# Optimization experiments

Hardware: AMD Instinct MI355X
Metric: run time of the kernel (lower is better)

Reference implementation:

```python
import jax, jax.numpy as jnp
import numpy as np
import math

D_MODEL = 1024
N_HEADS = 16
HEAD_DIM = D_MODEL // N_HEADS
WINDOW = 256
LN_EPS = 1e-5


def _layernorm(x, g, b):
    mu = jnp.mean(x, axis=-1, keepdims=True)
    var = jnp.var(x, axis=-1, keepdims=True)
    return (x - mu) * jax.lax.rsqrt(var + LN_EPS) * g + b


def _window_mask(L):
    # row i attends to columns [i - W//2, i + W//2] inclusive; -inf elsewhere
    i = jnp.arange(L)[:, None]
    j = jnp.arange(L)[None, :]
    inside = (j >= i - WINDOW // 2) & (j <= i + WINDOW // 2)
    return jnp.where(inside, 0.0, -jnp.inf)  # [L, L]


def setup_inputs() -> dict:
    key = jax.random.key(0)
    ks = jax.random.split(key, 6)
    B, L, D = 2, 2048, D_MODEL
    s = 0.02
    return {
        "x": jax.random.normal(ks[0], (B, L, D), jnp.float32),
        "qkv_w": jax.random.normal(ks[1], (D, 3 * D), jnp.float32) * s,
        "qkv_b": jnp.zeros((3 * D,), jnp.float32),
        "out_w": jax.random.normal(ks[2], (D, D), jnp.float32) * s,
        "out_b": jnp.zeros((D,), jnp.float32),
        "ln1_g": jnp.ones((D,), jnp.float32),
        "ln1_b": jnp.zeros((D,), jnp.float32),
        "ln2_g": jnp.ones((D,), jnp.float32),
        "ln2_b": jnp.zeros((D,), jnp.float32),
        "ffn_w1": jax.random.normal(ks[3], (D, 2 * D), jnp.float32) * s,
        "ffn_b1": jnp.zeros((2 * D,), jnp.float32),
        "ffn_w2": jax.random.normal(ks[4], (2 * D, D), jnp.float32) * s,
        "ffn_b2": jnp.zeros((D,), jnp.float32),
    }


def reference(x, qkv_w, qkv_b, out_w, out_b, ln1_g, ln1_b, ln2_g, ln2_b,
              ffn_w1, ffn_b1, ffn_w2, ffn_b2):
    B, L, D = x.shape
    # --- sparse (windowed) attention on LN1(x) ---
    h = _layernorm(x, ln1_g, ln1_b)
    qkv = h @ qkv_w + qkv_b                       # [B, L, 3D]
    qkv = qkv.reshape(B, L, 3, N_HEADS, HEAD_DIM)
    q = qkv[:, :, 0].transpose(0, 2, 1, 3)        # [B, H, L, hd]
    k = qkv[:, :, 1].transpose(0, 2, 1, 3)
    v = qkv[:, :, 2].transpose(0, 2, 1, 3)
    scores = jnp.einsum('bhqd,bhkd->bhqk', q, k) / math.sqrt(HEAD_DIM)
    scores = scores + _window_mask(L)             # broadcast [L,L] over [B,H]
    attn = jax.nn.softmax(scores, axis=-1)
    out = jnp.einsum('bhqk,bhkd->bhqd', attn, v)  # [B, H, L, hd]
    out = out.transpose(0, 2, 1, 3).reshape(B, L, D)
    attn_out = out @ out_w + out_b
    x = x + attn_out
    # --- FFN on LN2(x) ---
    h2 = _layernorm(x, ln2_g, ln2_b)
    ffn = jax.nn.gelu(h2 @ ffn_w1 + ffn_b1, approximate=False) @ ffn_w2 + ffn_b2
    return x + ffn
```

## Files before the change

### kernel.cpp

```cpp
#include <hip/hip_runtime.h>
#include <hip/hip_bf16.h>

#define D_MODEL 1024
#define L_SEQ   2048
#define BATCH   2
#define NROWS   (BATCH*L_SEQ)
#define N_HEADS 16
#define HD      64
#define WIN     128

typedef __attribute__((ext_vector_type(8))) short short8;
typedef __attribute__((ext_vector_type(4))) float f32x4;
typedef __attribute__((ext_vector_type(4))) int   i32x4;
typedef __attribute__((ext_vector_type(4))) unsigned short u16x4;

__device__ __forceinline__ float bf2f(unsigned short u) {
  union { unsigned int i; float f; } c;
  c.i = ((unsigned int)u) << 16;
  return c.f;
}
__device__ __forceinline__ unsigned short f2bf(float f) {
  __hip_bfloat16 h = __float2bfloat16(f);
  return *reinterpret_cast<unsigned short*>(&h);
}

__global__ __launch_bounds__(256) void wtrans_kernel(const float* __restrict__ W,
                                                     __hip_bfloat16* __restrict__ Wt,
                                                     int K, int N) {
  __shared__ float tile[32][33];
  int tx = threadIdx.x & 31, ty = threadIdx.x >> 5;
  int n0 = blockIdx.x * 32, k0 = blockIdx.y * 32;
#pragma unroll
  for (int i = 0; i < 4; ++i) {
    int k = k0 + ty + i * 8;
    tile[ty + i * 8][tx] = W[(size_t)k * N + n0 + tx];
  }
  __syncthreads();
#pragma unroll
  for (int i = 0; i < 4; ++i) {
    int n = n0 + ty + i * 8;
    Wt[(size_t)n * K + k0 + tx] = __float2bfloat16(tile[tx][ty + i * 8]);
  }
}

__global__ __launch_bounds__(256) void vtrans_kernel(const __hip_bfloat16* __restrict__ qkv,
                                                     __hip_bfloat16* __restrict__ vT) {
  __shared__ unsigned short tile[64][72];
  int bh = blockIdx.y, b = bh >> 4, h = bh & 15;
  int j0 = blockIdx.x * 64;
  int t = threadIdx.x;
#pragma unroll
  for (int i = 0; i < 2; ++i) {
    int c = t + i * 256;
    int row = c >> 3, off = c & 7;
    *(i32x4*)&tile[row][off * 8] =
        *(const i32x4*)&qkv[(size_t)(b * L_SEQ + j0 + row) * 3072 + 2 * D_MODEL + h * 64 + off * 8];
  }
  __syncthreads();
#pragma unroll
  for (int i = 0; i < 2; ++i) {
    int c = t + i * 256;
    int d = c >> 3, off = c & 7;
    short8 o;
#pragma unroll
    for (int e = 0; e < 8; ++e) o[e] = (short)tile[off * 8 + e][d];
    *(short8*)&vT[((size_t)bh * 64 + d) * 2048 + j0 + off * 8] = o;
  }
}

__global__ __launch_bounds__(256) void ln_kernel(const float* __restrict__ x,
                                                 const float* __restrict__ g,
                                                 const float* __restrict__ beta,
                                                 __hip_bfloat16* __restrict__ out) {
  int row = blockIdx.x;
  int t = threadIdx.x;
  const float4* xr = (const float4*)(x + (size_t)row * D_MODEL);
  float4 v = xr[t];
  float s  = v.x + v.y + v.z + v.w;
  float sq = v.x * v.x + v.y * v.y + v.z * v.z + v.w * v.w;
#pragma unroll
  for (int off = 32; off; off >>= 1) {
    s  += __shfl_xor(s, off);
    sq += __shfl_xor(sq, off);
  }
  __shared__ float red[8];
  int w = t >> 6;
  if ((t & 63) == 0) { red[w] = s; red[4 + w] = sq; }
  __syncthreads();
  s  = red[0] + red[1] + red[2] + red[3];
  sq = red[4] + red[5] + red[6] + red[7];
  float mean = s * (1.0f / 1024.0f);
  float var  = sq * (1.0f / 1024.0f) - mean * mean;
  float rs   = rsqrtf(var + 1e-5f);
  float4 gv = ((const float4*)g)[t];
  float4 bv = ((const float4*)beta)[t];
  u16x4 o;
  o.x = f2bf((v.x - mean) * rs * gv.x + bv.x);
  o.y = f2bf((v.y - mean) * rs * gv.y + bv.y);
  o.z = f2bf((v.z - mean) * rs * gv.z + bv.z);
  o.w = f2bf((v.w - mean) * rs * gv.w + bv.w);
  ((u16x4*)(out + (size_t)row * D_MODEL))[t] = o;
}

template <int MODE>
__global__ __launch_bounds__(256) void gemm_kernel(const __hip_bfloat16* __restrict__ A,
                                                   const __hip_bfloat16* __restrict__ Bt,
                                                   const float* __restrict__ bias,
                                                   const float* __restrict__ resid,
                                                   void* __restrict__ outp,
                                                   int M, int N, int K) {
  (void)M;
  __shared__ char lsA[128 * 128];
  __shared__ char lsB[128 * 128];

  int tid  = threadIdx.x;
  int lane = tid & 63;
  int wave = tid >> 6;
  int wr = wave >> 1, wc = wave & 1;

  int m0 = blockIdx.y * 128;
  int n0 = blockIdx.x * 128;

  const char* Abase = (const char*)A;
  const char* Bbase = (const char*)Bt;
  size_t strideK = (size_t)K * 2;
  int KT = K >> 6;

  int srow = tid >> 3;
  int skb  = (tid & 7) * 16;

  f32x4 zero = {0.f, 0.f, 0.f, 0.f};
  f32x4 acc[4][4];
#pragma unroll
  for (int i = 0; i < 4; ++i)
#pragma unroll
    for (int j = 0; j < 4; ++j) acc[i][j] = zero;

  i32x4 ra[4], rb[4];
#pragma unroll
  for (int c = 0; c < 4; ++c) {
    int row = srow + c * 32;
    ra[c] = *(const i32x4*)(Abase + (size_t)(m0 + row) * strideK + skb);
    rb[c] = *(const i32x4*)(Bbase + (size_t)(n0 + row) * strideK + skb);
  }
#pragma unroll
  for (int c = 0; c < 4; ++c) {
    int row = srow + c * 32;
    int kb  = skb ^ ((row & 7) << 4);
    *(i32x4*)(lsA + row * 128 + kb) = ra[c];
    *(i32x4*)(lsB + row * 128 + kb) = rb[c];
  }
  __syncthreads();

  for (int kt = 0; kt < KT; ++kt) {
    if (kt + 1 < KT) {
#pragma unroll
      for (int c = 0; c < 4; ++c) {
        int row = srow + c * 32;
        ra[c] = *(const i32x4*)(Abase + (size_t)(m0 + row) * strideK + (size_t)(kt + 1) * 128 + skb);
        rb[c] = *(const i32x4*)(Bbase + (size_t)(n0 + row) * strideK + (size_t)(kt + 1) * 128 + skb);
      }
    }
#pragma unroll
    for (int ks = 0; ks < 2; ++ks) {
      short8 af[4], bfr[4];
#pragma unroll
      for (int mi = 0; mi < 4; ++mi) {
        int row = wr * 64 + mi * 16 + (lane & 15);
        int kb  = (ks * 64 + ((lane >> 4) << 4)) ^ ((row & 7) << 4);
        af[mi] = *(const short8*)(lsA + row * 128 + kb);
      }
#pragma unroll
      for (int ni = 0; ni < 4; ++ni) {
        int row = wc * 64 + ni * 16 + (lane & 15);
        int kb  = (ks * 64 + ((lane >> 4) << 4)) ^ ((row & 7) << 4);
        bfr[ni] = *(const short8*)(lsB + row * 128 + kb);
      }
#pragma unroll
      for (int mi = 0; mi < 4; ++mi)
#pragma unroll
        for (int ni = 0; ni < 4; ++ni)
          acc[mi][ni] = __builtin_amdgcn_mfma_f32_16x16x32_bf16(af[mi], bfr[ni], acc[mi][ni], 0, 0, 0);
    }
    __syncthreads();
    if (kt + 1 < KT) {
#pragma unroll
      for (int c = 0; c < 4; ++c) {
        int row = srow + c * 32;
        int kb  = skb ^ ((row & 7) << 4);
        *(i32x4*)(lsA + row * 128 + kb) = ra[c];
        *(i32x4*)(lsB + row * 128 + kb) = rb[c];
      }
    }
    __syncthreads();
  }

  int colg = n0 + wc * 64;
  int rowg = m0 + wr * 64;
#pragma unroll
  for (int mi = 0; mi < 4; ++mi) {
#pragma unroll
    for (int ni = 0; ni < 4; ++ni) {
      int col = colg + ni * 16 + (lane & 15);
      float bs = bias[col];
#pragma unroll
      for (int r = 0; r < 4; ++r) {
        int row = rowg + mi * 16 + ((lane >> 4) << 2) + r;
        float v = acc[mi][ni][r] + bs;
        if (MODE == 1) v = 0.5f * v * (1.0f + erff(v * 0.70710678118654752f));
        if (MODE == 2) {
          ((float*)outp)[(size_t)row * N + col] = v + resid[(size_t)row * N + col];
        } else {
          ((__hip_bfloat16*)outp)[(size_t)row * N + col] = __float2bfloat16(v);
        }
      }
    }
  }
}

__global__ __launch_bounds__(256) void attn_mfma_kernel(const __hip_bfloat16* __restrict__ qkv,
                                                        const __hip_bfloat16* __restrict__ vT,
                                                        __hip_bfloat16* __restrict__ out) {
  __shared__ char Ks[2][8192];
  __shared__ char Vs[2][8192];
  __shared__ char Ps[4][2304];

  const int t = threadIdx.x;
  const int lane = t & 63;
  const int wave = t >> 6;
  const int l15 = lane & 15;
  const int lg  = lane >> 4;
  const int bh = blockIdx.y, b = bh >> 4, h = bh & 15;
  const int q0 = blockIdx.x * 64;
  const int jlo = q0 - 128;

  short8 qf0, qf1;
  {
    int qrow = q0 + wave * 16 + l15;
    const char* qp = (const char*)qkv + 2 * ((size_t)(b * L_SEQ + qrow) * 3072 + h * 64 + 8 * lg);
    qf0 = *(const short8*)qp;
    qf1 = *(const short8*)(qp + 64);
  }

  const int srow = t >> 3;
  const int soff = (t & 7) * 16;
  const int jel  = (t & 7) * 8;

  const char* kgbase = (const char*)qkv + 2 * ((size_t)b * L_SEQ * 3072 + D_MODEL + h * 64);
  const char* vgbase = (const char*)vT + 2 * ((size_t)bh * 64 * 2048);

  f32x4 sc[5][4];
#pragma unroll
  for (int c = 0; c < 5; ++c)
#pragma unroll
    for (int tt = 0; tt < 4; ++tt) sc[c][tt] = (f32x4){0.f, 0.f, 0.f, 0.f};

  {
    i32x4 kr[2];
#pragma unroll
    for (int i = 0; i < 2; ++i) {
      int rr = srow + i * 32;
      int tok = jlo + rr; tok = tok < 0 ? 0 : (tok > 2047 ? 2047 : tok);
      kr[i] = *(const i32x4*)(kgbase + (size_t)tok * 6144 + soff);
    }
#pragma unroll
    for (int i = 0; i < 2; ++i) {
      int rr = srow + i * 32;
      *(i32x4*)(Ks[0] + rr * 128 + (soff ^ ((rr & 7) << 4))) = kr[i];
    }
  }
  __syncthreads();

#pragma unroll
  for (int c = 0; c < 5; ++c) {
    int cur = c & 1;
    i32x4 nk[2];
    if (c < 4) {
#pragma unroll
      for (int i = 0; i < 2; ++i) {
        int rr = srow + i * 32;
        int tok = jlo + (c + 1) * 64 + rr; tok = tok < 0 ? 0 : (tok > 2047 ? 2047 : tok);
        nk[i] = *(const i32x4*)(kgbase + (size_t)tok * 6144 + soff);
      }
    }
#pragma unroll
    for (int tt = 0; tt < 4; ++tt) {
      int row = tt * 16 + l15;
      short8 k0 = *(const short8*)(Ks[cur] + row * 128 + ((lg * 16) ^ ((row & 7) << 4)));
      short8 k1 = *(const short8*)(Ks[cur] + row * 128 + ((64 + lg * 16) ^ ((row & 7) << 4)));
      sc[c][tt] = __builtin_amdgcn_mfma_f32_16x16x32_bf16(qf0, k0, sc[c][tt], 0, 0, 0);
      sc[c][tt] = __builtin_amdgcn_mfma_f32_16x16x32_bf16(qf1, k1, sc[c][tt], 0, 0, 0);
    }
    if (c < 4) {
      __syncthreads();
#pragma unroll
      for (int i = 0; i < 2; ++i) {
        int rr = srow + i * 32;
        *(i32x4*)(Ks[cur ^ 1] + rr * 128 + (soff ^ ((rr & 7) << 4))) = nk[i];
      }
      __syncthreads();
    }
  }

  const int iqb = q0 + wave * 16 + 4 * lg;
  const int kgb = jlo + l15;
#pragma unroll
  for (int c = 0; c < 5; ++c)
#pragma unroll
    for (int tt = 0; tt < 4; ++tt) {
      int kg = kgb + c * 64 + tt * 16;
#pragma unroll
      for (int r = 0; r < 4; ++r) {
        int iq = iqb + r;
        bool ok = (kg >= 0) && (kg < L_SEQ) && (kg >= iq - WIN) && (kg <= iq + WIN);
        sc[c][tt][r] = ok ? sc[c][tt][r] * 0.125f : -1e30f;
      }
    }
  float mx[4] = {-1e30f, -1e30f, -1e30f, -1e30f};
#pragma unroll
  for (int c = 0; c < 5; ++c)
#pragma unroll
    for (int tt = 0; tt < 4; ++tt)
#pragma unroll
      for (int r = 0; r < 4; ++r) mx[r] = fmaxf(mx[r], sc[c][tt][r]);
#pragma unroll
  for (int r = 0; r < 4; ++r)
#pragma unroll
    for (int off = 8; off; off >>= 1) mx[r] = fmaxf(mx[r], __shfl_xor(mx[r], off, 16));
  float sm[4] = {0.f, 0.f, 0.f, 0.f};
#pragma unroll
  for (int c = 0; c < 5; ++c)
#pragma unroll
    for (int tt = 0; tt < 4; ++tt)
#pragma unroll
      for (int r = 0; r < 4; ++r) {
        float p = __expf(sc[c][tt][r] - mx[r]);
        sc[c][tt][r] = p;
        sm[r] += p;
      }
#pragma unroll
  for (int r = 0; r < 4; ++r)
#pragma unroll
    for (int off = 8; off; off >>= 1) sm[r] += __shfl_xor(sm[r], off, 16);
  float inv[4];
#pragma unroll
  for (int r = 0; r < 4; ++r) inv[r] = 1.f / sm[r];
#pragma unroll
  for (int c = 0; c < 5; ++c)
#pragma unroll
    for (int tt = 0; tt < 4; ++tt)
#pragma unroll
      for (int r = 0; r < 4; ++r) sc[c][tt][r] *= inv[r];

  f32x4 o[4];
#pragma unroll
  for (int dt = 0; dt < 4; ++dt) o[dt] = (f32x4){0.f, 0.f, 0.f, 0.f};

  {
    i32x4 vr[2];
#pragma unroll
    for (int i = 0; i < 2; ++i) {
      int rr = srow + i * 32;
      int js = jlo + jel; js = js < 0 ? 0 : (js > 2040 ? 2040 : js);
      vr[i] = *(const i32x4*)(vgbase + 2 * ((size_t)rr * 2048 + js));
    }
    __syncthreads();
#pragma unroll
    for (int i = 0; i < 2; ++i) {
      int rr = srow + i * 32;
      *(i32x4*)(Vs[0] + rr * 128 + (soff ^ ((rr & 7) << 4))) = vr[i];
    }
  }
  __syncthreads();

  char* pw = Ps[wave];
#pragma unroll
  for (int c = 0; c < 5; ++c) {
    int cur = c & 1;
    i32x4 nv[2];
    if (c < 4) {
#pragma unroll
      for (int i = 0; i < 2; ++i) {
        int rr = srow + i * 32;
        int js = jlo + (c + 1) * 64 + jel; js = js < 0 ? 0 : (js > 2040 ? 2040 : js);
        nv[i] = *(const i32x4*)(vgbase + 2 * ((size_t)rr * 2048 + js));
      }
    }
#pragma unroll
    for (int tt = 0; tt < 4; ++tt)
#pragma unroll
      for (int r = 0; r < 4; ++r)
        *(unsigned short*)(pw + (4 * lg + r) * 144 + (tt * 16 + l15) * 2) = f2bf(sc[c][tt][r]);
    short8 pa0 = *(const short8*)(pw + l15 * 144 + lg * 16);
    short8 pa1 = *(const short8*)(pw + l15 * 144 + 64 + lg * 16);
#pragma unroll
    for (int dt = 0; dt < 4; ++dt) {
      int row = dt * 16 + l15;
      short8 v0 = *(const short8*)(Vs[cur] + row * 128 + ((lg * 16) ^ ((row & 7) << 4)));
      short8 v1 = *(const short8*)(Vs[cur] + row * 128 + ((64 + lg * 16) ^ ((row & 7) << 4)));
      o[dt] = __builtin_amdgcn_mfma_f32_16x16x32_bf16(pa0, v0, o[dt], 0, 0, 0);
      o[dt] = __builtin_amdgcn_mfma_f32_16x16x32_bf16(pa1, v1, o[dt], 0, 0, 0);
    }
    if (c < 4) {
      __syncthreads();
#pragma unroll
      for (int i = 0; i < 2; ++i) {
        int rr = srow + i * 32;
        *(i32x4*)(Vs[cur ^ 1] + rr * 128 + (soff ^ ((rr & 7) << 4))) = nv[i];
      }
      __syncthreads();
    }
  }

  char* ob = (char*)out + 2 * ((size_t)(b * L_SEQ + q0 + wave * 16) * D_MODEL + h * 64);
#pragma unroll
  for (int dt = 0; dt < 4; ++dt)
#pragma unroll
    for (int r = 0; r < 4; ++r)
      *(unsigned short*)(ob + 2 * ((size_t)(4 * lg + r) * D_MODEL + dt * 16 + l15)) = f2bf(o[dt][r]);
}

extern "C" void kernel_launch(void* const* d_in, const int* in_sizes, int n_in,
                              void* d_out, int out_size, void* d_ws, size_t ws_size,
                              hipStream_t stream) {
  const float* x      = (const float*)d_in[0];
  const float* qkv_w  = (const float*)d_in[1];
  const float* qkv_b  = (const float*)d_in[2];
  const float* out_w  = (const float*)d_in[3];
  const float* out_b  = (const float*)d_in[4];
  const float* ln1_g  = (const float*)d_in[5];
  const float* ln1_b  = (const float*)d_in[6];
  const float* ln2_g  = (const float*)d_in[7];
  const float* ln2_b  = (const float*)d_in[8];
  const float* ffn_w1 = (const float*)d_in[9];
  const float* ffn_b1 = (const float*)d_in[10];
  const float* ffn_w2 = (const float*)d_in[11];
  const float* ffn_b2 = (const float*)d_in[12];
  float* out = (float*)d_out;
  (void)in_sizes; (void)n_in; (void)out_size; (void)ws_size;

  char* ws = (char*)d_ws;
  size_t off = 0;
  auto alloc = [&](size_t bytes) {
    char* p = ws + off;
    off += (bytes + 255) & ~(size_t)255;
    return p;
  };
  __hip_bfloat16* hbuf    = (__hip_bfloat16*)alloc((size_t)NROWS * 1024 * 2);
  __hip_bfloat16* qkvbuf  = (__hip_bfloat16*)alloc((size_t)NROWS * 3072 * 2);
  __hip_bfloat16* attnbuf = (__hip_bfloat16*)alloc((size_t)NROWS * 1024 * 2);
  float*          x2buf   = (float*)alloc((size_t)NROWS * 1024 * 4);
  __hip_bfloat16* wqkvT   = (__hip_bfloat16*)alloc((size_t)3072 * 1024 * 2);
  __hip_bfloat16* woutT   = (__hip_bfloat16*)alloc((size_t)1024 * 1024 * 2);
  __hip_bfloat16* wf1T    = (__hip_bfloat16*)alloc((size_t)2048 * 1024 * 2);
  __hip_bfloat16* wf2T    = (__hip_bfloat16*)alloc((size_t)1024 * 2048 * 2);
  __hip_bfloat16* vTbuf   = (__hip_bfloat16*)alloc((size_t)32 * 64 * 2048 * 2);
  __hip_bfloat16* gbuf    = qkvbuf;

  dim3 blk(256);
  wtrans_kernel<<<dim3(3072 / 32, 1024 / 32), blk, 0, stream>>>(qkv_w, wqkvT, 1024, 3072);
  wtrans_kernel<<<dim3(1024 / 32, 1024 / 32), blk, 0, stream>>>(out_w, woutT, 1024, 1024);
  wtrans_kernel<<<dim3(2048 / 32, 1024 / 32), blk, 0, stream>>>(ffn_w1, wf1T, 1024, 2048);
  wtrans_kernel<<<dim3(1024 / 32, 2048 / 32), blk, 0, stream>>>(ffn_w2, wf2T, 2048, 1024);

  ln_kernel<<<NROWS, blk, 0, stream>>>(x, ln1_g, ln1_b, hbuf);
  gemm_kernel<0><<<dim3(3072 / 128, NROWS / 128), blk, 0, stream>>>(hbuf, wqkvT, qkv_b, nullptr, qkvbuf, NROWS, 3072, 1024);
  vtrans_kernel<<<dim3(L_SEQ / 64, BATCH * N_HEADS), blk, 0, stream>>>(qkvbuf, vTbuf);
  attn_mfma_kernel<<<dim3(L_SEQ / 64, BATCH * N_HEADS), blk, 0, stream>>>(qkvbuf, vTbuf, attnbuf);
  gemm_kernel<2><<<dim3(1024 / 128, NROWS / 128), blk, 0, stream>>>(attnbuf, woutT, out_b, x, x2buf, NROWS, 1024, 1024);
  ln_kernel<<<NROWS, blk, 0, stream>>>(x2buf, ln2_g, ln2_b, hbuf);
  gemm_kernel<1><<<dim3(2048 / 128, NROWS / 128), blk, 0, stream>>>(hbuf, wf1T, ffn_b1, nullptr, gbuf, NROWS, 2048, 1024);
  gemm_kernel<2><<<dim3(1024 / 128, NROWS / 128), blk, 0, stream>>>(gbuf, wf2T, ffn_b2, x2buf, out, NROWS, 1024, 2048);
}
```

Measured before the change: 259.5 us.

## Fuse weight transposes with LN1 and stage GEMM tiles via global_load_lds

```diff
diff --git a/kernel.cpp b/kernel.cpp
--- a/kernel.cpp
+++ b/kernel.cpp
@@ -24,12 +24,18 @@
   return *reinterpret_cast<unsigned short*>(&h);
 }
 
-__global__ __launch_bounds__(256) void wtrans_kernel(const float* __restrict__ W,
-                                                     __hip_bfloat16* __restrict__ Wt,
-                                                     int K, int N) {
+__device__ __forceinline__ void gload16(const void* g, void* l) {
+  __builtin_amdgcn_global_load_lds((const __attribute__((address_space(1))) unsigned int*)g,
+                                   (__attribute__((address_space(3))) unsigned int*)l, 16, 0, 0);
+}
+
+__device__ __forceinline__ void wtrans_body(const float* __restrict__ W,
+                                            __hip_bfloat16* __restrict__ Wt,
+                                            int K, int N, int tile_id) {
   __shared__ float tile[32][33];
   int tx = threadIdx.x & 31, ty = threadIdx.x >> 5;
-  int n0 = blockIdx.x * 32, k0 = blockIdx.y * 32;
+  int ntile_n = N >> 5;
+  int n0 = (tile_id % ntile_n) * 32, k0 = (tile_id / ntile_n) * 32;
 #pragma unroll
   for (int i = 0; i < 4; ++i) {
     int k = k0 + ty + i * 8;
@@ -43,36 +49,10 @@
   }
 }
 
-__global__ __launch_bounds__(256) void vtrans_kernel(const __hip_bfloat16* __restrict__ qkv,
-                                                     __hip_bfloat16* __restrict__ vT) {
-  __shared__ unsigned short tile[64][72];
-  int bh = blockIdx.y, b = bh >> 4, h = bh & 15;
-  int j0 = blockIdx.x * 64;
-  int t = threadIdx.x;
-#pragma unroll
-  for (int i = 0; i < 2; ++i) {
-    int c = t + i * 256;
-    int row = c >> 3, off = c & 7;
-    *(i32x4*)&tile[row][off * 8] =
-        *(const i32x4*)&qkv[(size_t)(b * L_SEQ + j0 + row) * 3072 + 2 * D_MODEL + h * 64 + off * 8];
-  }
-  __syncthreads();
-#pragma unroll
-  for (int i = 0; i < 2; ++i) {
-    int c = t + i * 256;
-    int d = c >> 3, off = c & 7;
-    short8 o;
-#pragma unroll
-    for (int e = 0; e < 8; ++e) o[e] = (short)tile[off * 8 + e][d];
-    *(short8*)&vT[((size_t)bh * 64 + d) * 2048 + j0 + off * 8] = o;
-  }
-}
-
-__global__ __launch_bounds__(256) void ln_kernel(const float* __restrict__ x,
-                                                 const float* __restrict__ g,
-                                                 const float* __restrict__ beta,
-                                                 __hip_bfloat16* __restrict__ out) {
-  int row = blockIdx.x;
+__device__ __forceinline__ void ln_body(const float* __restrict__ x,
+                                        const float* __restrict__ g,
+                                        const float* __restrict__ beta,
+                                        __hip_bfloat16* __restrict__ out, int row) {
   int t = threadIdx.x;
   const float4* xr = (const float4*)(x + (size_t)row * D_MODEL);
   float4 v = xr[t];
@@ -102,6 +82,53 @@
   ((u16x4*)(out + (size_t)row * D_MODEL))[t] = o;
 }
 
+__global__ __launch_bounds__(256) void prep_kernel(
+    const float* __restrict__ qkv_w, __hip_bfloat16* __restrict__ wqkvT,
+    const float* __restrict__ out_w, __hip_bfloat16* __restrict__ woutT,
+    const float* __restrict__ ffn_w1, __hip_bfloat16* __restrict__ wf1T,
+    const float* __restrict__ ffn_w2, __hip_bfloat16* __restrict__ wf2T,
+    const float* __restrict__ x, const float* __restrict__ ln1_g,
+    const float* __restrict__ ln1_b, __hip_bfloat16* __restrict__ hbuf) {
+  int id = blockIdx.x;
+  if (id < 3072)      wtrans_body(qkv_w,  wqkvT, 1024, 3072, id);
+  else if (id < 4096) wtrans_body(out_w,  woutT, 1024, 1024, id - 3072);
+  else if (id < 6144) wtrans_body(ffn_w1, wf1T,  1024, 2048, id - 4096);
+  else if (id < 8192) wtrans_body(ffn_w2, wf2T,  2048, 1024, id - 6144);
+  else                ln_body(x, ln1_g, ln1_b, hbuf, id - 8192);
+}
+
+__global__ __launch_bounds__(256) void ln_kernel(const float* __restrict__ x,
+                                                 const float* __restrict__ g,
+                                                 const float* __restrict__ beta,
+                                                 __hip_bfloat16* __restrict__ out) {
+  ln_body(x, g, beta, out, blockIdx.x);
+}
+
+__global__ __launch_bounds__(256) void vtrans_kernel(const __hip_bfloat16* __restrict__ qkv,
+                                                     __hip_bfloat16* __restrict__ vT) {
+  __shared__ unsigned short tile[64][72];
+  int bh = blockIdx.y, b = bh >> 4, h = bh & 15;
+  int j0 = blockIdx.x * 64;
+  int t = threadIdx.x;
+#pragma unroll
+  for (int i = 0; i < 2; ++i) {
+    int c = t + i * 256;
+    int row = c >> 3, off = c & 7;
+    *(i32x4*)&tile[row][off * 8] =
+        *(const i32x4*)&qkv[(size_t)(b * L_SEQ + j0 + row) * 3072 + 2 * D_MODEL + h * 64 + off * 8];
+  }
+  __syncthreads();
+#pragma unroll
+  for (int i = 0; i < 2; ++i) {
+    int c = t + i * 256;
+    int d = c >> 3, off = c & 7;
+    short8 o;
+#pragma unroll
+    for (int e = 0; e < 8; ++e) o[e] = (short)tile[off * 8 + e][d];
+    *(short8*)&vT[((size_t)bh * 64 + d) * 2048 + j0 + off * 8] = o;
+  }
+}
+
 template <int MODE>
 __global__ __launch_bounds__(256) void gemm_kernel(const __hip_bfloat16* __restrict__ A,
                                                    const __hip_bfloat16* __restrict__ Bt,
@@ -110,13 +137,14 @@
                                                    void* __restrict__ outp,
                                                    int M, int N, int K) {
   (void)M;
-  __shared__ char lsA[128 * 128];
-  __shared__ char lsB[128 * 128];
+  __shared__ __align__(16) char lsA[128 * 128];
+  __shared__ __align__(16) char lsB[128 * 128];
 
   int tid  = threadIdx.x;
   int lane = tid & 63;
   int wave = tid >> 6;
   int wr = wave >> 1, wc = wave & 1;
+  int l15 = lane & 15, lg = lane >> 4;
 
   int m0 = blockIdx.y * 128;
   int n0 = blockIdx.x * 128;
@@ -126,8 +154,8 @@
   size_t strideK = (size_t)K * 2;
   int KT = K >> 6;
 
-  int srow = tid >> 3;
-  int skb  = (tid & 7) * 16;
+  int srow_in = lane >> 3;
+  int scb     = (lane & 7) * 16;
 
   f32x4 zero = {0.f, 0.f, 0.f, 0.f};
   f32x4 acc[4][4];
@@ -136,45 +164,28 @@
 #pragma unroll
     for (int j = 0; j < 4; ++j) acc[i][j] = zero;
 
-  i32x4 ra[4], rb[4];
-#pragma unroll
-  for (int c = 0; c < 4; ++c) {
-    int row = srow + c * 32;
-    ra[c] = *(const i32x4*)(Abase + (size_t)(m0 + row) * strideK + skb);
-    rb[c] = *(const i32x4*)(Bbase + (size_t)(n0 + row) * strideK + skb);
-  }
-#pragma unroll
-  for (int c = 0; c < 4; ++c) {
-    int row = srow + c * 32;
-    int kb  = skb ^ ((row & 7) << 4);
-    *(i32x4*)(lsA + row * 128 + kb) = ra[c];
-    *(i32x4*)(lsB + row * 128 + kb) = rb[c];
-  }
-  __syncthreads();
-
   for (int kt = 0; kt < KT; ++kt) {
-    if (kt + 1 < KT) {
-#pragma unroll
-      for (int c = 0; c < 4; ++c) {
-        int row = srow + c * 32;
-        ra[c] = *(const i32x4*)(Abase + (size_t)(m0 + row) * strideK + (size_t)(kt + 1) * 128 + skb);
-        rb[c] = *(const i32x4*)(Bbase + (size_t)(n0 + row) * strideK + (size_t)(kt + 1) * 128 + skb);
-      }
-    }
+    size_t kb = (size_t)kt * 128;
+#pragma unroll
+    for (int i = 0; i < 4; ++i) {
+      int chunk = wave * 4 + i;
+      int row = chunk * 8 + srow_in;
+      gload16(Abase + (size_t)(m0 + row) * strideK + kb + scb, lsA + chunk * 1024);
+      gload16(Bbase + (size_t)(n0 + row) * strideK + kb + scb, lsB + chunk * 1024);
+    }
+    __syncthreads();
 #pragma unroll
     for (int ks = 0; ks < 2; ++ks) {
       short8 af[4], bfr[4];
 #pragma unroll
       for (int mi = 0; mi < 4; ++mi) {
-        int row = wr * 64 + mi * 16 + (lane & 15);
-        int kb  = (ks * 64 + ((lane >> 4) << 4)) ^ ((row & 7) << 4);
-        af[mi] = *(const short8*)(lsA + row * 128 + kb);
+        int row = wr * 64 + mi * 16 + l15;
+        af[mi] = *(const short8*)(lsA + row * 128 + ks * 64 + lg * 16);
       }
 #pragma unroll
       for (int ni = 0; ni < 4; ++ni) {
-        int row = wc * 64 + ni * 16 + (lane & 15);
-        int kb  = (ks * 64 + ((lane >> 4) << 4)) ^ ((row & 7) << 4);
-        bfr[ni] = *(const short8*)(lsB + row * 128 + kb);
+        int row = wc * 64 + ni * 16 + l15;
+        bfr[ni] = *(const short8*)(lsB + row * 128 + ks * 64 + lg * 16);
       }
 #pragma unroll
       for (int mi = 0; mi < 4; ++mi)
@@ -183,16 +194,6 @@
           acc[mi][ni] = __builtin_amdgcn_mfma_f32_16x16x32_bf16(af[mi], bfr[ni], acc[mi][ni], 0, 0, 0);
     }
     __syncthreads();
-    if (kt + 1 < KT) {
-#pragma unroll
-      for (int c = 0; c < 4; ++c) {
-        int row = srow + c * 32;
-        int kb  = skb ^ ((row & 7) << 4);
-        *(i32x4*)(lsA + row * 128 + kb) = ra[c];
-        *(i32x4*)(lsB + row * 128 + kb) = rb[c];
-      }
-    }
-    __syncthreads();
   }
 
   int colg = n0 + wc * 64;
@@ -201,11 +202,11 @@
   for (int mi = 0; mi < 4; ++mi) {
 #pragma unroll
     for (int ni = 0; ni < 4; ++ni) {
-      int col = colg + ni * 16 + (lane & 15);
+      int col = colg + ni * 16 + l15;
       float bs = bias[col];
 #pragma unroll
       for (int r = 0; r < 4; ++r) {
-        int row = rowg + mi * 16 + ((lane >> 4) << 2) + r;
+        int row = rowg + mi * 16 + (lg << 2) + r;
         float v = acc[mi][ni][r] + bs;
         if (MODE == 1) v = 0.5f * v * (1.0f + erff(v * 0.70710678118654752f));
         if (MODE == 2) {
@@ -458,12 +459,9 @@
   __hip_bfloat16* gbuf    = qkvbuf;
 
   dim3 blk(256);
-  wtrans_kernel<<<dim3(3072 / 32, 1024 / 32), blk, 0, stream>>>(qkv_w, wqkvT, 1024, 3072);
-  wtrans_kernel<<<dim3(1024 / 32, 1024 / 32), blk, 0, stream>>>(out_w, woutT, 1024, 1024);
-  wtrans_kernel<<<dim3(2048 / 32, 1024 / 32), blk, 0, stream>>>(ffn_w1, wf1T, 1024, 2048);
-  wtrans_kernel<<<dim3(1024 / 32, 2048 / 32), blk, 0, stream>>>(ffn_w2, wf2T, 2048, 1024);
-
-  ln_kernel<<<NROWS, blk, 0, stream>>>(x, ln1_g, ln1_b, hbuf);
+  prep_kernel<<<8192 + NROWS, blk, 0, stream>>>(qkv_w, wqkvT, out_w, woutT,
+                                                ffn_w1, wf1T, ffn_w2, wf2T,
+                                                x, ln1_g, ln1_b, hbuf);
   gemm_kernel<0><<<dim3(3072 / 128, NROWS / 128), blk, 0, stream>>>(hbuf, wqkvT, qkv_b, nullptr, qkvbuf, NROWS, 3072, 1024);
   vtrans_kernel<<<dim3(L_SEQ / 64, BATCH * N_HEADS), blk, 0, stream>>>(qkvbuf, vTbuf);
   attn_mfma_kernel<<<dim3(L_SEQ / 64, BATCH * N_HEADS), blk, 0, stream>>>(qkvbuf, vTbuf, attnbuf);
```

Result: slower. 301.9 us (+16.3%).
